# Optimization experiments

Hardware: AMD Instinct MI355X
Metric: run time of the kernel (lower is better)

## Reference

```python
import jax, jax.numpy as jnp
import numpy as np

N, C, G, M, E = 100000, 8, 8, 32, 1600000
EPS = 1e-8


def setup_inputs() -> dict:
    key = jax.random.key(0)
    k1, k2, k3, k4, k5 = jax.random.split(key, 5)
    x = jax.random.randint(k1, (N,), 0, M)
    prev_h = jax.random.uniform(k2, (N, C, G), dtype=jnp.float32)
    edge_index = jax.random.randint(k3, (2, E), 0, N)
    Q_neigh = jax.random.normal(k4, (C, C, G), dtype=jnp.float32) * 1.25
    B = jax.random.normal(k5, (C, M, G), dtype=jnp.float32) * 1.25
    return {"x": x, "prev_h": prev_h, "edge_index": edge_index,
            "Q_neigh": Q_neigh, "B": B}


def reference(x, prev_h, edge_index, Q_neigh, B):
    n = prev_h.shape[0]
    # softmax reparameterization (vectorized over n_gen)
    Qs = jax.nn.softmax(Q_neigh, axis=0)          # [C, C, G], columns sum to 1 over dim 0
    Bs = jax.nn.softmax(B, axis=1)                # [C, M, G], rows sum to 1 over M

    dst, src = edge_index[0], edge_index[1]
    neigh = prev_h[src]                            # [E, C, G] gather
    summed = jax.ops.segment_sum(neigh, dst, num_segments=n)            # [N, C, G]
    counts = jax.ops.segment_sum(jnp.ones((src.shape[0],), prev_h.dtype), dst,
                                 num_segments=n)                        # [N]
    aggr = summed / jnp.maximum(counts, 1.0)[:, None, None]             # scatter-mean, 0 for isolated nodes

    B_nodes = jnp.transpose(Bs[:, x], (1, 0, 2))[:, :, None, :]         # [N, C, 1, G]
    unnorm = B_nodes * (Qs[None, :, :, :] * aggr[:, None, :, :]) + EPS  # [N, C, C, G]

    denom = unnorm.sum(axis=(1, 2), keepdims=True)                      # [N, 1, 1, G]
    posterior_il = unnorm / denom
    posterior_i = posterior_il.sum(axis=2)                              # [N, C, G]
    likelihood = jnp.log(jnp.squeeze(denom, (1, 2)))                    # [N, G]
    return likelihood, posterior_i
```

## Files before the change

kernel.cpp:

```cpp
#include <hip/hip_runtime.h>

#define C_    8
#define G_    8
#define CG    64
#define CAP   48
#define CELL  56
#define BSPAN 256
#define SBLK  256
#define CVT   160
#define Z1    768
#define Z2    768
#define ZTOT  4096
#define EPSF  1e-8f

__device__ __forceinline__ unsigned short bf16rne(float v) {
    unsigned u = __float_as_uint(v);
    return (unsigned short)((u + 0x7FFFu + ((u >> 16) & 1u)) >> 16);
}
__device__ __forceinline__ float bf16tof(unsigned short h) {
    return __uint_as_float((unsigned)h << 16);
}

__device__ __forceinline__ void zsum_block(int zgid, const float* __restrict__ Bmat,
                                           float* __restrict__ Z, int M) {
    if (zgid >= ZTOT) return;
    __shared__ float zpart[4][8];
    int c = zgid & 7, bx = zgid >> 3;
    const float4* B4 = (const float4*)(Bmat + (size_t)c * M * G_);
    const int total4 = M * 2;
    int tid = bx * 256 + threadIdx.x;
    const int zstride = (ZTOT / 8) * 256;
    float a0 = 0.f, a1 = 0.f, a2 = 0.f, a3 = 0.f;
    for (int f = tid; f < total4; f += zstride) {
        float4 v = B4[f];
        a0 += __expf(v.x); a1 += __expf(v.y); a2 += __expf(v.z); a3 += __expf(v.w);
    }
    #pragma unroll
    for (int m = 2; m <= 32; m <<= 1) {
        a0 += __shfl_xor(a0, m, 64);
        a1 += __shfl_xor(a1, m, 64);
        a2 += __shfl_xor(a2, m, 64);
        a3 += __shfl_xor(a3, m, 64);
    }
    int lane = threadIdx.x & 63, w = threadIdx.x >> 6;
    if (lane < 2) {
        int g0 = lane * 4;
        zpart[w][g0 + 0] = a0; zpart[w][g0 + 1] = a1;
        zpart[w][g0 + 2] = a2; zpart[w][g0 + 3] = a3;
    }
    __syncthreads();
    if (threadIdx.x < 8) {
        float s = zpart[0][threadIdx.x] + zpart[1][threadIdx.x]
                + zpart[2][threadIdx.x] + zpart[3][threadIdx.x];
        atomicAdd(&Z[c * G_ + threadIdx.x], s);
    }
}

__global__ void k_d1(const int* __restrict__ ei, int E, int npart,
                     int* __restrict__ counts, int* __restrict__ staging,
                     const float* __restrict__ prev_h, unsigned short* __restrict__ ph16,
                     int N, const float* __restrict__ Qn, float* __restrict__ Qs,
                     const float* __restrict__ Bmat, float* __restrict__ Z, int M) {
    int b = blockIdx.x;
    if (b < SBLK) {
        __shared__ int cur[512];
        for (int p = threadIdx.x; p < npart; p += 256) cur[p] = 0;
        __syncthreads();
        int chunk = (E + SBLK - 1) / SBLK;
        int lo = b * chunk, hi = min(E, lo + chunk);
        for (int e = lo + threadIdx.x; e < hi; e += 256) {
            int dst = ei[e], src = ei[E + e];
            int p = dst >> 8;
            int c = atomicAdd(&cur[p], 1);
            if (c < CELL) staging[(p * SBLK + b) * CELL + c] = ((dst & 255) << 23) | src;
        }
        __syncthreads();
        for (int p = threadIdx.x; p < npart; p += 256)
            counts[p * SBLK + b] = cur[p];
    } else if (b < SBLK + CVT) {
        int gid = (b - SBLK) * 256 + threadIdx.x;
        int total8 = N * 8;
        const int cstride = CVT * 256;
        for (int f = gid; f < total8; f += cstride) {
            const float4* s = (const float4*)(prev_h + (size_t)f * 8);
            float4 v0 = s[0], v1 = s[1];
            float vv[8] = {v0.x, v0.y, v0.z, v0.w, v1.x, v1.y, v1.z, v1.w};
            unsigned r[4];
            #pragma unroll
            for (int k = 0; k < 4; ++k)
                r[k] = (unsigned)bf16rne(vv[2 * k]) | ((unsigned)bf16rne(vv[2 * k + 1]) << 16);
            *(uint4*)(ph16 + (size_t)f * 8) = make_uint4(r[0], r[1], r[2], r[3]);
        }
    } else if (b == SBLK + CVT) {
        __shared__ float e[512];
        __shared__ float cs[64];
        int t = threadIdx.x;
        e[t] = __expf(Qn[t]); e[t + 256] = __expf(Qn[t + 256]);
        __syncthreads();
        if (t < 64) {
            float s = 0.f;
            #pragma unroll
            for (int i2 = 0; i2 < 8; ++i2) s += e[i2 * 64 + t];
            cs[t] = s;
        }
        __syncthreads();
        Qs[t] = e[t] / cs[t & 63];
        Qs[t + 256] = e[t + 256] / cs[t & 63];
    } else {
        zsum_block(b - (SBLK + CVT + 1), Bmat, Z, M);
    }
}

__global__ void k_d2(const int* __restrict__ counts, const int* __restrict__ staging,
                     int* __restrict__ cnt, int* __restrict__ csr, int N, int npart,
                     const float* __restrict__ Bmat, float* __restrict__ Z, int M) {
    int b = blockIdx.x;
    if (b >= npart) { zsum_block(Z1 + (b - npart), Bmat, Z, M); return; }
    __shared__ int cl[BSPAN];
    __shared__ int csl[BSPAN * CAP];
    int t = threadIdx.x;
    cl[t] = 0;
    __syncthreads();
    int cnum = min(counts[b * SBLK + t], CELL);
    int cbase = (b * SBLK + t) * CELL;
    for (int j = 0; j < cnum; ++j) {
        int v = staging[cbase + j];
        int local = (unsigned)v >> 23;
        int src = v & 0x7FFFFF;
        int pos = atomicAdd(&cl[local], 1);
        if (pos < CAP) csl[local * CAP + pos] = src;
    }
    __syncthreads();
    int n = b * BSPAN + t;
    if (n < N) cnt[n] = cl[t];
    for (int idx = t; idx < BSPAN * CAP; idx += 256)
        csr[(size_t)b * (BSPAN * CAP) + idx] = csl[idx];
}

__global__ void k_ti(const unsigned short* __restrict__ ph16, const int* __restrict__ cnt,
                     const int* __restrict__ csr, const float* __restrict__ Qs,
                     unsigned short* __restrict__ ti16, const int* __restrict__ x,
                     const float* __restrict__ Bmat, unsigned short* __restrict__ blog16,
                     float* __restrict__ Z, int M, int N, int ngroups) {
    int grp = blockIdx.x / 13, r = blockIdx.x % 13;
    int lane = threadIdx.x & 63, w = threadIdx.x >> 6;
    int i = lane >> 3, g = lane & 7;
    if (r < 8) {
        int a = grp * 8 + r;
        int base = a * 16 + w * 4;
        if (base >= N) return;
        int nk[4]; bool valid[4]; int deg[4], dl[4], nb[4];
        #pragma unroll
        for (int k = 0; k < 4; ++k) {
            int n = base + k;
            valid[k] = (n < N);
            nk[k] = valid[k] ? n : (N - 1);
        }
        #pragma unroll
        for (int k = 0; k < 4; ++k) {
            deg[k] = valid[k] ? cnt[nk[k]] : 0;
            dl[k]  = min(deg[k], CAP);
            nb[k]  = dl[k] >> 2;
        }
        float q[8];
        #pragma unroll
        for (int l = 0; l < 8; ++l) q[l] = Qs[i * 64 + l * 8 + g];
        float acc[4] = {0.f, 0.f, 0.f, 0.f};
        int nbmax = max(max(nb[0], nb[1]), max(nb[2], nb[3]));
        for (int q2 = 0; q2 < nbmax; ++q2) {
            #pragma unroll
            for (int k = 0; k < 4; ++k) {
                if (q2 < nb[k]) {
                    int4 s4 = ((const int4*)(csr + (size_t)nk[k] * CAP))[q2];
                    acc[k] += bf16tof(ph16[(s4.x << 6) | lane]);
                    acc[k] += bf16tof(ph16[(s4.y << 6) | lane]);
                    acc[k] += bf16tof(ph16[(s4.z << 6) | lane]);
                    acc[k] += bf16tof(ph16[(s4.w << 6) | lane]);
                }
            }
        }
        #pragma unroll
        for (int k = 0; k < 4; ++k) {
            const int* crow = csr + (size_t)nk[k] * CAP;
            for (int e2 = nb[k] * 4; e2 < dl[k]; ++e2)
                acc[k] += bf16tof(ph16[(crow[e2] << 6) | lane]);
        }
        #pragma unroll
        for (int k = 0; k < 4; ++k) {
            float aggr = (deg[k] > 0) ? acc[k] / (float)deg[k] : 0.f;
            float ti = 0.f;
            #pragma unroll
            for (int l = 0; l < 8; ++l) ti += q[l] * __shfl(aggr, l * 8 + g, 64);
            if (valid[k]) ti16[(size_t)nk[k] * CG + lane] = bf16rne(ti);
        }
    } else if (r == 8) {
        const int step = ngroups * 16;
        for (int n0 = (grp * 4 + w) * 4; n0 < N; n0 += step) {
            int xs[4];
            #pragma unroll
            for (int k = 0; k < 4; ++k) xs[k] = (n0 + k < N) ? x[n0 + k] : 0;
            #pragma unroll
            for (int k = 0; k < 4; ++k)
                if (n0 + k < N)
                    blog16[(size_t)(n0 + k) * CG + lane] =
                        bf16rne(Bmat[((size_t)i * M + xs[k]) * G_ + g]);
        }
    } else {
        zsum_block(Z1 + Z2 + grp * 4 + (r - 9), Bmat, Z, M);
    }
}

__global__ void k_epi(const unsigned short* __restrict__ ti16,
                      const unsigned short* __restrict__ blog16,
                      const float* __restrict__ Z, float* __restrict__ out, int N) {
    int w = threadIdx.x >> 6, lane = threadIdx.x & 63;
    int i = lane >> 3, g = lane & 7;
    int base = (blockIdx.x * 4 + w) * 4;
    if (base >= N) return;
    float invZ = 1.f / Z[lane];
    #pragma unroll
    for (int k = 0; k < 4; ++k) {
        int n = base + k;
        if (n >= N) break;
        float ti = bf16tof(ti16[(size_t)n * CG + lane]);
        float bl = bf16tof(blog16[(size_t)n * CG + lane]);
        float u = __expf(bl) * invZ * ti;
        float s = u;
        #pragma unroll
        for (int m = 8; m <= 32; m <<= 1) s += __shfl_xor(s, m, 64);
        float denom = s + 64.f * EPSF;
        if (i == 0) out[n * G_ + g] = logf(denom);
        out[(size_t)N * G_ + (size_t)n * CG + lane] = (u + 8.f * EPSF) / denom;
    }
}

extern "C" void kernel_launch(void* const* d_in, const int* in_sizes, int n_in,
                              void* d_out, int out_size, void* d_ws, size_t ws_size,
                              hipStream_t stream) {
    const int*   x      = (const int*)d_in[0];
    const float* prev_h = (const float*)d_in[1];
    const int*   ei     = (const int*)d_in[2];
    const float* Qn     = (const float*)d_in[3];
    const float* Bm     = (const float*)d_in[4];
    float* out = (float*)d_out;

    int N = in_sizes[0];
    int E = in_sizes[2] / 2;
    int M = in_sizes[4] / CG;
    int npart = (N + BSPAN - 1) / BSPAN;

    int nblk16  = (N + 15) / 16;
    int ngroups = (nblk16 + 7) / 8;
    int zg      = (ZTOT - Z1 - Z2 + 3) / 4;
    if (ngroups < zg) ngroups = zg;

    float* Z      = (float*)d_ws;
    float* Qs     = Z + 64;
    int*   counts = (int*)d_ws + 576;
    int*   cnt    = counts + npart * SBLK;
    int*   stag   = cnt + N;
    int*   csr    = stag + (size_t)npart * SBLK * CELL;
    unsigned short* ph16   = (unsigned short*)(csr + (size_t)npart * BSPAN * CAP);
    unsigned short* blog16 = ph16 + (size_t)N * CG;
    unsigned short* ti16   = blog16 + (size_t)N * CG;

    hipMemsetAsync(d_ws, 0, 64 * sizeof(float), stream);

    k_d1<<<SBLK + CVT + 1 + Z1, 256, 0, stream>>>(ei, E, npart, counts, stag,
                                                  prev_h, ph16, N, Qn, Qs, Bm, Z, M);
    k_d2<<<npart + Z2, 256, 0, stream>>>(counts, stag, cnt, csr, N, npart, Bm, Z, M);
    k_ti<<<ngroups * 13, 256, 0, stream>>>(ph16, cnt, csr, Qs, ti16, x, Bm, blog16,
                                           Z, M, N, ngroups);
    k_epi<<<(N + 15) / 16, 256, 0, stream>>>(ti16, blog16, Z, out, N);
}
```

Measured before the change: 139.3 us.

## Move B-row gather to first kernel and rebalance Z-sum blocks across launches

The gather of B rows into blog16, which depends only on x and B, moves from the aggregation kernel into the first kernel as 512 extra blocks. There it runs alongside the edge bucketing and bf16 conversion. The column-sum blocks for Z are redistributed across the three launches (more in k_d1 and k_d2, fewer in k_ti). The aggregation kernel now uses a simple linear block index in place of the 13-way interleaved grouping. The aim is to shorten the critical aggregation kernel by moving independent work into earlier kernels, at the cost of making those earlier kernels larger.

```diff
diff --git a/kernel.cpp b/kernel.cpp
--- a/kernel.cpp
+++ b/kernel.cpp
@@ -8,8 +8,9 @@
 #define BSPAN 256
 #define SBLK  256
 #define CVT   160
-#define Z1    768
-#define Z2    768
+#define BG    512
+#define Z1    1720
+#define Z2    1280
 #define ZTOT  4096
 #define EPSF  1e-8f
 
@@ -60,6 +61,7 @@
                      int* __restrict__ counts, int* __restrict__ staging,
                      const float* __restrict__ prev_h, unsigned short* __restrict__ ph16,
                      int N, const float* __restrict__ Qn, float* __restrict__ Qs,
+                     const int* __restrict__ x, unsigned short* __restrict__ blog16,
                      const float* __restrict__ Bmat, float* __restrict__ Z, int M) {
     int b = blockIdx.x;
     if (b < SBLK) {
@@ -106,8 +108,23 @@
         __syncthreads();
         Qs[t] = e[t] / cs[t & 63];
         Qs[t + 256] = e[t + 256] / cs[t & 63];
+    } else if (b < SBLK + CVT + 1 + BG) {
+        int gidx = b - (SBLK + CVT + 1);
+        int lane = threadIdx.x & 63, w = threadIdx.x >> 6;
+        int i = lane >> 3, g = lane & 7;
+        const int step = BG * 4 * 4;
+        for (int n0 = (gidx * 4 + w) * 4; n0 < N; n0 += step) {
+            int xs[4];
+            #pragma unroll
+            for (int k = 0; k < 4; ++k) xs[k] = (n0 + k < N) ? x[n0 + k] : 0;
+            #pragma unroll
+            for (int k = 0; k < 4; ++k)
+                if (n0 + k < N)
+                    blog16[(size_t)(n0 + k) * CG + lane] =
+                        bf16rne(Bmat[((size_t)i * M + xs[k]) * G_ + g]);
+        }
     } else {
-        zsum_block(b - (SBLK + CVT + 1), Bmat, Z, M);
+        zsum_block(b - (SBLK + CVT + 1 + BG), Bmat, Z, M);
     }
 }
 
@@ -139,74 +156,58 @@
 
 __global__ void k_ti(const unsigned short* __restrict__ ph16, const int* __restrict__ cnt,
                      const int* __restrict__ csr, const float* __restrict__ Qs,
-                     unsigned short* __restrict__ ti16, const int* __restrict__ x,
-                     const float* __restrict__ Bmat, unsigned short* __restrict__ blog16,
-                     float* __restrict__ Z, int M, int N, int ngroups) {
-    int grp = blockIdx.x / 13, r = blockIdx.x % 13;
+                     unsigned short* __restrict__ ti16,
+                     const float* __restrict__ Bmat, float* __restrict__ Z,
+                     int M, int N, int nAggr) {
+    int b = blockIdx.x;
+    if (b >= nAggr) { zsum_block(Z1 + Z2 + (b - nAggr), Bmat, Z, M); return; }
     int lane = threadIdx.x & 63, w = threadIdx.x >> 6;
     int i = lane >> 3, g = lane & 7;
-    if (r < 8) {
-        int a = grp * 8 + r;
-        int base = a * 16 + w * 4;
-        if (base >= N) return;
-        int nk[4]; bool valid[4]; int deg[4], dl[4], nb[4];
+    int base = b * 16 + w * 4;
+    if (base >= N) return;
+    int nk[4]; bool valid[4]; int deg[4], dl[4], nb[4];
+    #pragma unroll
+    for (int k = 0; k < 4; ++k) {
+        int n = base + k;
+        valid[k] = (n < N);
+        nk[k] = valid[k] ? n : (N - 1);
+    }
+    #pragma unroll
+    for (int k = 0; k < 4; ++k) {
+        deg[k] = valid[k] ? cnt[nk[k]] : 0;
+        dl[k]  = min(deg[k], CAP);
+        nb[k]  = dl[k] >> 2;
+    }
+    float q[8];
+    #pragma unroll
+    for (int l = 0; l < 8; ++l) q[l] = Qs[i * 64 + l * 8 + g];
+    float acc[4] = {0.f, 0.f, 0.f, 0.f};
+    int nbmax = max(max(nb[0], nb[1]), max(nb[2], nb[3]));
+    for (int q2 = 0; q2 < nbmax; ++q2) {
         #pragma unroll
         for (int k = 0; k < 4; ++k) {
-            int n = base + k;
-            valid[k] = (n < N);
-            nk[k] = valid[k] ? n : (N - 1);
-        }
+            if (q2 < nb[k]) {
+                int4 s4 = ((const int4*)(csr + (size_t)nk[k] * CAP))[q2];
+                acc[k] += bf16tof(ph16[(s4.x << 6) | lane]);
+                acc[k] += bf16tof(ph16[(s4.y << 6) | lane]);
+                acc[k] += bf16tof(ph16[(s4.z << 6) | lane]);
+                acc[k] += bf16tof(ph16[(s4.w << 6) | lane]);
+            }
+        }
+    }
+    #pragma unroll
+    for (int k = 0; k < 4; ++k) {
+        const int* crow = csr + (size_t)nk[k] * CAP;
+        for (int e2 = nb[k] * 4; e2 < dl[k]; ++e2)
+            acc[k] += bf16tof(ph16[(crow[e2] << 6) | lane]);
+    }
+    #pragma unroll
+    for (int k = 0; k < 4; ++k) {
+        float aggr = (deg[k] > 0) ? acc[k] / (float)deg[k] : 0.f;
+        float ti = 0.f;
         #pragma unroll
-        for (int k = 0; k < 4; ++k) {
-            deg[k] = valid[k] ? cnt[nk[k]] : 0;
-            dl[k]  = min(deg[k], CAP);
-            nb[k]  = dl[k] >> 2;
-        }
-        float q[8];
-        #pragma unroll
-        for (int l = 0; l < 8; ++l) q[l] = Qs[i * 64 + l * 8 + g];
-        float acc[4] = {0.f, 0.f, 0.f, 0.f};
-        int nbmax = max(max(nb[0], nb[1]), max(nb[2], nb[3]));
-        for (int q2 = 0; q2 < nbmax; ++q2) {
-            #pragma unroll
-            for (int k = 0; k < 4; ++k) {
-                if (q2 < nb[k]) {
-                    int4 s4 = ((const int4*)(csr + (size_t)nk[k] * CAP))[q2];
-                    acc[k] += bf16tof(ph16[(s4.x << 6) | lane]);
-                    acc[k] += bf16tof(ph16[(s4.y << 6) | lane]);
-                    acc[k] += bf16tof(ph16[(s4.z << 6) | lane]);
-                    acc[k] += bf16tof(ph16[(s4.w << 6) | lane]);
-                }
-            }
-        }
-        #pragma unroll
-        for (int k = 0; k < 4; ++k) {
-            const int* crow = csr + (size_t)nk[k] * CAP;
-            for (int e2 = nb[k] * 4; e2 < dl[k]; ++e2)
-                acc[k] += bf16tof(ph16[(crow[e2] << 6) | lane]);
-        }
-        #pragma unroll
-        for (int k = 0; k < 4; ++k) {
-            float aggr = (deg[k] > 0) ? acc[k] / (float)deg[k] : 0.f;
-            float ti = 0.f;
-            #pragma unroll
-            for (int l = 0; l < 8; ++l) ti += q[l] * __shfl(aggr, l * 8 + g, 64);
-            if (valid[k]) ti16[(size_t)nk[k] * CG + lane] = bf16rne(ti);
-        }
-    } else if (r == 8) {
-        const int step = ngroups * 16;
-        for (int n0 = (grp * 4 + w) * 4; n0 < N; n0 += step) {
-            int xs[4];
-            #pragma unroll
-            for (int k = 0; k < 4; ++k) xs[k] = (n0 + k < N) ? x[n0 + k] : 0;
-            #pragma unroll
-            for (int k = 0; k < 4; ++k)
-                if (n0 + k < N)
-                    blog16[(size_t)(n0 + k) * CG + lane] =
-                        bf16rne(Bmat[((size_t)i * M + xs[k]) * G_ + g]);
-        }
-    } else {
-        zsum_block(Z1 + Z2 + grp * 4 + (r - 9), Bmat, Z, M);
+        for (int l = 0; l < 8; ++l) ti += q[l] * __shfl(aggr, l * 8 + g, 64);
+        if (valid[k]) ti16[(size_t)nk[k] * CG + lane] = bf16rne(ti);
     }
 }
 
@@ -248,11 +249,7 @@
     int E = in_sizes[2] / 2;
     int M = in_sizes[4] / CG;
     int npart = (N + BSPAN - 1) / BSPAN;
-
-    int nblk16  = (N + 15) / 16;
-    int ngroups = (nblk16 + 7) / 8;
-    int zg      = (ZTOT - Z1 - Z2 + 3) / 4;
-    if (ngroups < zg) ngroups = zg;
+    int nAggr = (N + 15) / 16;
 
     float* Z      = (float*)d_ws;
     float* Qs     = Z + 64;
@@ -266,10 +263,10 @@
 
     hipMemsetAsync(d_ws, 0, 64 * sizeof(float), stream);
 
-    k_d1<<<SBLK + CVT + 1 + Z1, 256, 0, stream>>>(ei, E, npart, counts, stag,
-                                                  prev_h, ph16, N, Qn, Qs, Bm, Z, M);
+    k_d1<<<SBLK + CVT + 1 + BG + Z1, 256, 0, stream>>>(
+        ei, E, npart, counts, stag, prev_h, ph16, N, Qn, Qs, x, blog16, Bm, Z, M);
     k_d2<<<npart + Z2, 256, 0, stream>>>(counts, stag, cnt, csr, N, npart, Bm, Z, M);
-    k_ti<<<ngroups * 13, 256, 0, stream>>>(ph16, cnt, csr, Qs, ti16, x, Bm, blog16,
-                                           Z, M, N, ngroups);
+    k_ti<<<nAggr + (ZTOT - Z1 - Z2), 256, 0, stream>>>(ph16, cnt, csr, Qs, ti16,
+                                                       Bm, Z, M, N, nAggr);
     k_epi<<<(N + 15) / 16, 256, 0, stream>>>(ti16, blog16, Z, out, N);
 }
```

New measurement: 145.3 us. +4.3%, slower.
